# Performance work log

Hardware: AMD Instinct MI355X
Metric: run time of the kernel (lower is better)

The kernel has to match this reference:

```python
import jax, jax.numpy as jnp
import numpy as np
jax.config.update("jax_enable_x64", True)

HASH_PRIMES = [2654435761, 2246822519, 3266489917, 2028178513, 1220703125, 1610612741, 805306457, 402653189, 3674653429, 2860486313, 1073676287, 2971215073, 1500450271, 3267000013, 2654435789, 4049292737, 2246822531, 3266489927, 2028178519, 1220703133, 1610612743, 805306459, 402653191, 3674653433]
NUM_TABLES = 32
BUCKETS = 4096
VOCAB = 1024
BYTE_DIM = 256
EMBED_PER_TABLE = 8
HIDDEN = 512
N_BLOCKS = 3  # num_layers - 1
BATCH, SEQ = 32, 2048

def _generate_skip_patterns(num_tables):
    patterns = []
    for offset in range(1, min(num_tables // 4 + 1, 9)):
        patterns.append((offset,))
    pairs = [(1,2),(2,3),(3,4),(1,3),(2,4),(1,4),(1,5),(2,5),(3,5),(1,6),(2,6),(1,7)]
    for p in pairs:
        if len(patterns) >= num_tables:
            break
        patterns.append(p)
    trigrams = [(1,2,3),(1,2,4),(1,3,5),(2,3,4),(1,2,5),(1,3,4),(2,4,6),(1,4,7)]
    for t in trigrams:
        if len(patterns) >= num_tables:
            break
        patterns.append(t)
    offset = 8
    while len(patterns) < num_tables:
        patterns.append((1, offset))
        offset += 1
    return tuple(patterns[:num_tables])

SKIP_PATTERNS = _generate_skip_patterns(NUM_TABLES)

def _soft_hash(tokens, table_idx):
    # tokens: [B,S] int64. Faithful to torch: h = h ^ (shifted*prime);
    # h2 = h ^ ((h*prime2) >> 16)  (python precedence: * > >> > ^)
    B, S = tokens.shape
    pattern = SKIP_PATTERNS[table_idx]
    h = jnp.zeros((B, S), dtype=jnp.int64)
    for k, offset in enumerate(pattern):
        prime = HASH_PRIMES[(table_idx * 3 + k) % len(HASH_PRIMES)]
        shifted = jnp.zeros_like(tokens)
        if offset < S:
            shifted = shifted.at[:, offset:].set(tokens[:, :S - offset])
        h = h ^ (shifted * jnp.int64(prime))
    idx_lo = h % BUCKETS
    sp = HASH_PRIMES[(table_idx * 3 + len(pattern)) % len(HASH_PRIMES)]
    h2 = h ^ ((h * jnp.int64(sp)) >> 16)
    idx_hi = h2 % BUCKETS
    frac = (((h >> 3) & 255).astype(jnp.float32) / 255.0) * 0.4
    return idx_lo, idx_hi, frac

def setup_inputs() -> dict:
    key = jax.random.key(0)
    ks = jax.random.split(key, 8)
    chars = jax.random.randint(ks[0], (BATCH, SEQ), 0, VOCAB, dtype=jnp.int64)
    byte_embed = jax.random.normal(ks[1], (VOCAB, BYTE_DIM), dtype=jnp.float32)
    hash_tables = 0.02 * jax.random.normal(ks[2], (NUM_TABLES, BUCKETS, EMBED_PER_TABLE), dtype=jnp.float32)
    s_in = float(np.sqrt(6.0 / (HIDDEN + HIDDEN)))
    w_in = jax.random.uniform(ks[3], (HIDDEN, HIDDEN), jnp.float32, -s_in, s_in)
    b_in = jnp.zeros((HIDDEN,), jnp.float32)
    mlp_ws = jax.random.uniform(ks[4], (N_BLOCKS, HIDDEN, HIDDEN), jnp.float32, -s_in, s_in)
    mlp_bs = jnp.zeros((N_BLOCKS, HIDDEN), jnp.float32)
    s_out = float(np.sqrt(6.0 / (HIDDEN + VOCAB)))
    w_out = jax.random.uniform(ks[5], (VOCAB, HIDDEN), jnp.float32, -s_out, s_out)
    b_out = jnp.zeros((VOCAB,), jnp.float32)
    return {"chars": chars, "byte_embed": byte_embed, "hash_tables": hash_tables,
            "w_in": w_in, "b_in": b_in, "mlp_ws": mlp_ws, "mlp_bs": mlp_bs,
            "w_out": w_out, "b_out": b_out}

def reference(chars, byte_embed, hash_tables, w_in, b_in, mlp_ws, mlp_bs, w_out, b_out):
    # chars: [B,S] int64 -> logits [B,S,V]
    parts = [byte_embed[chars]]  # [B,S,256]
    for i in range(NUM_TABLES):
        idx_lo, idx_hi, frac = _soft_hash(chars, i)
        tab = hash_tables[i]                      # [BUCKETS, 8]
        frac = frac[..., None]                    # [B,S,1]
        emb = tab[idx_lo] * (1.0 - frac) + tab[idx_hi] * frac
        parts.append(emb)
    features = jnp.concatenate(parts, axis=-1)    # [B,S,512]
    h = jax.nn.relu(features @ w_in.T + b_in)
    for j in range(N_BLOCKS):
        # ResidualBlock: relu(linear(x)) + x (no layernorm/dropout in config)
        h = jax.nn.relu(h @ mlp_ws[j].T + mlp_bs[j]) + h
    logits = h @ w_out.T + b_out                  # [B,S,VOCAB]
    return logits
```

## Files before the change

### kernel.cpp

```cpp
#include <hip/hip_runtime.h>
#include <cstdint>
#include <cstddef>

typedef unsigned short u16;
typedef __attribute__((ext_vector_type(8))) short short8;
typedef __attribute__((ext_vector_type(4))) float f32x4;

#define NTOK 65536
#define HID 512
#define NVOCAB 1024

__device__ __forceinline__ u16 f2bf(float f) {
  union { float f; uint32_t u; } v; v.f = f;
  uint32_t r = (v.u + 0x7FFFu + ((v.u >> 16) & 1u)) >> 16;
  return (u16)r;
}
__device__ __forceinline__ float bf2f(u16 b) {
  union { uint32_t u; float f; } v; v.u = ((uint32_t)b) << 16;
  return v.f;
}

__constant__ uint32_t P24[24] = {
  2654435761u, 2246822519u, 3266489917u, 2028178513u, 1220703125u,
  1610612741u, 805306457u, 402653189u, 3674653429u, 2860486313u,
  1073676287u, 2971215073u, 1500450271u, 3267000013u, 2654435789u,
  4049292737u, 2246822531u, 3266489927u, 2028178519u, 1220703133u,
  1610612743u, 805306459u, 402653191u, 3674653433u};
__constant__ unsigned char OFFS[32][3] = {
  {1,0,0},{2,0,0},{3,0,0},{4,0,0},{5,0,0},{6,0,0},{7,0,0},{8,0,0},
  {1,2,0},{2,3,0},{3,4,0},{1,3,0},{2,4,0},{1,4,0},{1,5,0},{2,5,0},
  {3,5,0},{1,6,0},{2,6,0},{1,7,0},
  {1,2,3},{1,2,4},{1,3,5},{2,3,4},{1,2,5},{1,3,4},{2,4,6},{1,4,7},
  {1,8,0},{1,9,0},{1,10,0},{1,11,0}};
__constant__ unsigned char PLEN[32] = {
  1,1,1,1,1,1,1,1, 2,2,2,2,2,2,2,2,2,2,2,2, 3,3,3,3,3,3,3,3, 2,2,2,2};

__global__ __launch_bounds__(256) void pack_w(
    const float* __restrict__ w_in, const float* __restrict__ mlp_ws,
    const float* __restrict__ w_out, u16* __restrict__ Wp)
{
  const int gid  = blockIdx.x * 256 + threadIdx.x;
  const int L    = gid >> 15;
  const int c    = gid & 32767;
  const int lane = c & 63;
  const int ni   = (c >> 6) & 3;
  const int kk   = (c >> 8) & 15;
  const int w    = c >> 12;
  const float* base =
      (L == 0) ? w_in :
      (L <= 3) ? mlp_ws + (size_t)(L - 1) * 262144 :
                 w_out  + (size_t)(L - 4) * 262144;
  const int row = (w << 6) + (ni << 4) + (lane & 15);
  const int col = (kk << 5) + ((lane >> 4) << 3);
  const float* s = base + (size_t)row * 512 + col;
  float4 f0 = ((const float4*)s)[0];
  float4 f1 = ((const float4*)s)[1];
  short8 o;
  o[0]=(short)f2bf(f0.x); o[1]=(short)f2bf(f0.y); o[2]=(short)f2bf(f0.z); o[3]=(short)f2bf(f0.w);
  o[4]=(short)f2bf(f1.x); o[5]=(short)f2bf(f1.y); o[6]=(short)f2bf(f1.z); o[7]=(short)f2bf(f1.w);
  *(short8*)(Wp + (size_t)gid * 8) = o;
}

__global__ __launch_bounds__(512, 4)
void fused_all(const int* __restrict__ chars, const float* __restrict__ byte_embed,
               const float* __restrict__ hash_tables, const u16* __restrict__ Wp,
               const float* __restrict__ bIn, const float* __restrict__ bMlp,
               const float* __restrict__ bOut, float* __restrict__ out)
{
  __shared__ __align__(16) u16 hbuf[64 * 512];
  const int tid  = threadIdx.x;
  const int w    = tid >> 6;
  const int lane = tid & 63;
  const int g    = lane >> 4;
  const int lr   = lane & 15;
  const size_t tok0 = (size_t)blockIdx.x << 6;
  const int swz = (lr & 7) << 3;

  {
    const int sub = tid & 31;
    const int tl  = tid >> 5;
    const int i   = sub;
    const int pl  = (int)PLEN[i];
    #pragma unroll 1
    for (int pass = 0; pass < 4; ++pass) {
      const int tr = (pass << 4) + tl;
      const size_t t = tok0 + tr;
      const int pos = (int)(t & 2047);
      const int c = chars[t];
      const int sw = (tr & 7) << 3;
      {
        const float* src = byte_embed + ((size_t)c << 8) + (sub << 3);
        float4 f0 = ((const float4*)src)[0];
        float4 f1 = ((const float4*)src)[1];
        short8 o;
        o[0]=(short)f2bf(f0.x); o[1]=(short)f2bf(f0.y); o[2]=(short)f2bf(f0.z); o[3]=(short)f2bf(f0.w);
        o[4]=(short)f2bf(f1.x); o[5]=(short)f2bf(f1.y); o[6]=(short)f2bf(f1.z); o[7]=(short)f2bf(f1.w);
        *(short8*)&hbuf[(tr << 9) + (((sub << 3)) ^ sw)] = o;
      }
      {
        long long hv = 0;
        #pragma unroll
        for (int k = 0; k < 3; ++k) {
          if (k < pl) {
            const int off = (int)OFFS[i][k];
            const long long tok = (pos >= off) ? (long long)chars[t - off] : 0ll;
            hv ^= tok * (long long)P24[(3 * i + k) % 24];
          }
        }
        const int idx_lo = (int)(hv & 4095);
        const long long p2 = (long long)P24[(3 * i + pl) % 24];
        const long long prod = (long long)((unsigned long long)hv * (unsigned long long)p2);
        const long long h2 = hv ^ (prod >> 16);
        const int idx_hi = (int)(h2 & 4095);
        const float frac = ((float)(int)((hv >> 3) & 255) / 255.0f) * 0.4f;
        const float om = 1.0f - frac;
        const float* plo = hash_tables + (((size_t)i << 12) + (size_t)idx_lo) * 8;
        const float* phi = hash_tables + (((size_t)i << 12) + (size_t)idx_hi) * 8;
        float4 a0 = ((const float4*)plo)[0], a1 = ((const float4*)plo)[1];
        float4 b0 = ((const float4*)phi)[0], b1 = ((const float4*)phi)[1];
        short8 o;
        o[0]=(short)f2bf(a0.x*om + b0.x*frac); o[1]=(short)f2bf(a0.y*om + b0.y*frac);
        o[2]=(short)f2bf(a0.z*om + b0.z*frac); o[3]=(short)f2bf(a0.w*om + b0.w*frac);
        o[4]=(short)f2bf(a1.x*om + b1.x*frac); o[5]=(short)f2bf(a1.y*om + b1.y*frac);
        o[6]=(short)f2bf(a1.z*om + b1.z*frac); o[7]=(short)f2bf(a1.w*om + b1.w*frac);
        *(short8*)&hbuf[(tr << 9) + (((256 + (sub << 3))) ^ sw)] = o;
      }
    }
  }
  __syncthreads();

  f32x4 acc[4][4];

  auto gemm = [&](int L) {
    #pragma unroll
    for (int ni = 0; ni < 4; ++ni)
      #pragma unroll
      for (int ti = 0; ti < 4; ++ti) acc[ni][ti] = (f32x4){0.f, 0.f, 0.f, 0.f};
    const u16* Wl = Wp + (size_t)L * 262144 + (w << 15) + (lane << 3);
    #pragma unroll
    for (int kk = 0; kk < 16; ++kk) {
      short8 Wf[4], hf[4];
      #pragma unroll
      for (int ni = 0; ni < 4; ++ni)
        Wf[ni] = *(const short8*)(Wl + (kk << 11) + (ni << 9));
      const int kb = ((kk << 5) + (g << 3)) ^ swz;
      #pragma unroll
      for (int ti = 0; ti < 4; ++ti)
        hf[ti] = *(const short8*)&hbuf[(((ti << 4) + lr) << 9) + kb];
      #pragma unroll
      for (int ni = 0; ni < 4; ++ni)
        #pragma unroll
        for (int ti = 0; ti < 4; ++ti)
          acc[ni][ti] = __builtin_amdgcn_mfma_f32_16x16x32_bf16(Wf[ni], hf[ti], acc[ni][ti], 0, 0, 0);
    }
  };

  auto epi_h = [&](const float* __restrict__ bias, bool resid) {
    __syncthreads();
    #pragma unroll
    for (int ni = 0; ni < 4; ++ni) {
      const int nb = (w << 6) + (ni << 4) + (g << 2);
      const float4 b4 = *(const float4*)(bias + nb);
      #pragma unroll
      for (int ti = 0; ti < 4; ++ti) {
        const int t = (ti << 4) + lr;
        u16* p = &hbuf[(t << 9) + (nb ^ swz)];
        float v0 = fmaxf(acc[ni][ti][0] + b4.x, 0.f);
        float v1 = fmaxf(acc[ni][ti][1] + b4.y, 0.f);
        float v2 = fmaxf(acc[ni][ti][2] + b4.z, 0.f);
        float v3 = fmaxf(acc[ni][ti][3] + b4.w, 0.f);
        if (resid) {
          const uint2 r2 = *(const uint2*)p;
          v0 += bf2f((u16)(r2.x & 0xffffu)); v1 += bf2f((u16)(r2.x >> 16));
          v2 += bf2f((u16)(r2.y & 0xffffu)); v3 += bf2f((u16)(r2.y >> 16));
        }
        uint2 o;
        o.x = (uint32_t)f2bf(v0) | ((uint32_t)f2bf(v1) << 16);
        o.y = (uint32_t)f2bf(v2) | ((uint32_t)f2bf(v3) << 16);
        *(uint2*)p = o;
      }
    }
    __syncthreads();
  };

  auto epi_out = [&](const float* __restrict__ bias, int vb) {
    #pragma unroll
    for (int ni = 0; ni < 4; ++ni) {
      const int nb = (w << 6) + (ni << 4) + (g << 2);
      const float4 b4 = *(const float4*)(bias + nb);
      #pragma unroll
      for (int ti = 0; ti < 4; ++ti) {
        const int t = (ti << 4) + lr;
        float4 o;
        o.x = acc[ni][ti][0] + b4.x;
        o.y = acc[ni][ti][1] + b4.y;
        o.z = acc[ni][ti][2] + b4.z;
        o.w = acc[ni][ti][3] + b4.w;
        *(float4*)(out + (tok0 + t) * NVOCAB + vb + nb) = o;
      }
    }
  };

  gemm(0); epi_h(bIn, false);
  gemm(1); epi_h(bMlp,        true);
  gemm(2); epi_h(bMlp + 512,  true);
  gemm(3); epi_h(bMlp + 1024, true);
  gemm(4); epi_out(bOut,       0);
  gemm(5); epi_out(bOut + 512, 512);
}

extern "C" void kernel_launch(void* const* d_in, const int* in_sizes, int n_in,
                              void* d_out, int out_size, void* d_ws, size_t ws_size,
                              hipStream_t stream) {
  const int*   chars      = (const int*)  d_in[0];
  const float* byte_embed = (const float*)d_in[1];
  const float* hash_tabs  = (const float*)d_in[2];
  const float* w_in       = (const float*)d_in[3];
  const float* b_in       = (const float*)d_in[4];
  const float* mlp_ws     = (const float*)d_in[5];
  const float* mlp_bs     = (const float*)d_in[6];
  const float* w_out      = (const float*)d_in[7];
  const float* b_out      = (const float*)d_in[8];

  u16* Wp = (u16*)d_ws;

  pack_w<<<dim3(768), dim3(256), 0, stream>>>(w_in, mlp_ws, w_out, Wp);

  fused_all<<<dim3(NTOK / 64), dim3(512), 0, stream>>>(
      chars, byte_embed, hash_tabs, Wp, b_in, mlp_bs, b_out, (float*)d_out);
}
```

Measured before the change: 525.1 us.

## Persistent 1024-thread blocks with double-buffered feature prefetch overlapping GEMMs

Switches to 256 persistent blocks of 1024 threads, each handling four 64-token tiles. The feature gather for the next tile goes into a second LDS buffer while the output GEMMs of the current tile run. Each wave now owns 32 output columns instead of 64, and the weight packing layout is changed to match. MFMA sections are wrapped in s_setprio. The aim is to hide gather latency and raise wave count per CU, at the cost of 128KB of LDS per block, one block per CU, and less weight reuse per wave.

```diff
diff --git a/kernel.cpp b/kernel.cpp
--- a/kernel.cpp
+++ b/kernel.cpp
@@ -43,14 +43,14 @@
   const int L    = gid >> 15;
   const int c    = gid & 32767;
   const int lane = c & 63;
-  const int ni   = (c >> 6) & 3;
-  const int kk   = (c >> 8) & 15;
-  const int w    = c >> 12;
+  const int ni   = (c >> 6) & 1;
+  const int kk   = (c >> 7) & 15;
+  const int w    = c >> 11;
   const float* base =
       (L == 0) ? w_in :
       (L <= 3) ? mlp_ws + (size_t)(L - 1) * 262144 :
                  w_out  + (size_t)(L - 4) * 262144;
-  const int row = (w << 6) + (ni << 4) + (lane & 15);
+  const int row = (w << 5) + (ni << 4) + (lane & 15);
   const int col = (kk << 5) + ((lane >> 4) << 3);
   const float* s = base + (size_t)row * 512 + col;
   float4 f0 = ((const float4*)s)[0];
@@ -61,132 +61,128 @@
   *(short8*)(Wp + (size_t)gid * 8) = o;
 }
 
-__global__ __launch_bounds__(512, 4)
+__global__ __launch_bounds__(1024, 4)
 void fused_all(const int* __restrict__ chars, const float* __restrict__ byte_embed,
                const float* __restrict__ hash_tables, const u16* __restrict__ Wp,
                const float* __restrict__ bIn, const float* __restrict__ bMlp,
                const float* __restrict__ bOut, float* __restrict__ out)
 {
-  __shared__ __align__(16) u16 hbuf[64 * 512];
+  __shared__ __align__(16) u16 hh[2][64 * 512];
   const int tid  = threadIdx.x;
   const int w    = tid >> 6;
   const int lane = tid & 63;
   const int g    = lane >> 4;
   const int lr   = lane & 15;
-  const size_t tok0 = (size_t)blockIdx.x << 6;
-  const int swz = (lr & 7) << 3;
-
-  {
-    const int sub = tid & 31;
-    const int tl  = tid >> 5;
-    const int i   = sub;
-    const int pl  = (int)PLEN[i];
-    #pragma unroll 1
-    for (int pass = 0; pass < 4; ++pass) {
-      const int tr = (pass << 4) + tl;
-      const size_t t = tok0 + tr;
-      const int pos = (int)(t & 2047);
-      const int c = chars[t];
-      const int sw = (tr & 7) << 3;
-      {
-        const float* src = byte_embed + ((size_t)c << 8) + (sub << 3);
-        float4 f0 = ((const float4*)src)[0];
-        float4 f1 = ((const float4*)src)[1];
-        short8 o;
-        o[0]=(short)f2bf(f0.x); o[1]=(short)f2bf(f0.y); o[2]=(short)f2bf(f0.z); o[3]=(short)f2bf(f0.w);
-        o[4]=(short)f2bf(f1.x); o[5]=(short)f2bf(f1.y); o[6]=(short)f2bf(f1.z); o[7]=(short)f2bf(f1.w);
-        *(short8*)&hbuf[(tr << 9) + (((sub << 3)) ^ sw)] = o;
+  const int swz  = (lr & 7) << 3;
+  const int sub  = tid & 31;
+  const int tl   = tid >> 5;
+  const int pl   = (int)PLEN[sub];
+
+  f32x4 acc[2][4];
+  float4 G0, G1, G2, G3, G4, G5;
+  float  frS;
+
+  auto feat_issue = [&](size_t tok0t, int p) {
+    const int tr = (p << 5) + tl;
+    const size_t t = tok0t + tr;
+    const int pos = (int)(t & 2047);
+    const int c = chars[t];
+    long long hv = 0;
+    #pragma unroll
+    for (int k = 0; k < 3; ++k) {
+      if (k < pl) {
+        const int off = (int)OFFS[sub][k];
+        const long long tok = (pos >= off) ? (long long)chars[t - off] : 0ll;
+        hv ^= tok * (long long)P24[(3 * sub + k) % 24];
       }
-      {
-        long long hv = 0;
+    }
+    const int idx_lo = (int)(hv & 4095);
+    const long long sp = (long long)P24[(3 * sub + pl) % 24];
+    const long long prod = (long long)((unsigned long long)hv * (unsigned long long)sp);
+    const int idx_hi = (int)((hv ^ (prod >> 16)) & 4095);
+    frS = ((float)(int)((hv >> 3) & 255) / 255.0f) * 0.4f;
+    const float* plo = hash_tables + (((size_t)sub << 12) + (size_t)idx_lo) * 8;
+    const float* phi = hash_tables + (((size_t)sub << 12) + (size_t)idx_hi) * 8;
+    const float* pby = byte_embed + ((size_t)c << 8) + (sub << 3);
+    G0 = ((const float4*)plo)[0]; G1 = ((const float4*)plo)[1];
+    G2 = ((const float4*)phi)[0]; G3 = ((const float4*)phi)[1];
+    G4 = ((const float4*)pby)[0]; G5 = ((const float4*)pby)[1];
+  };
+  auto feat_consume = [&](u16* hb, int p) {
+    const int tr = (p << 5) + tl;
+    const int sw = (tr & 7) << 3;
+    short8 ob;
+    ob[0]=(short)f2bf(G4.x); ob[1]=(short)f2bf(G4.y); ob[2]=(short)f2bf(G4.z); ob[3]=(short)f2bf(G4.w);
+    ob[4]=(short)f2bf(G5.x); ob[5]=(short)f2bf(G5.y); ob[6]=(short)f2bf(G5.z); ob[7]=(short)f2bf(G5.w);
+    *(short8*)&hb[(tr << 9) + ((sub << 3) ^ sw)] = ob;
+    const float fr = frS, om = 1.0f - fr;
+    short8 oh;
+    oh[0]=(short)f2bf(G0.x*om + G2.x*fr); oh[1]=(short)f2bf(G0.y*om + G2.y*fr);
+    oh[2]=(short)f2bf(G0.z*om + G2.z*fr); oh[3]=(short)f2bf(G0.w*om + G2.w*fr);
+    oh[4]=(short)f2bf(G1.x*om + G3.x*fr); oh[5]=(short)f2bf(G1.y*om + G3.y*fr);
+    oh[6]=(short)f2bf(G1.z*om + G3.z*fr); oh[7]=(short)f2bf(G1.w*om + G3.w*fr);
+    *(short8*)&hb[(tr << 9) + ((256 + (sub << 3)) ^ sw)] = oh;
+  };
+
+  auto gemm = [&](int L, const u16* hb, int kk0, int kk1, bool zero) {
+    if (zero) {
+      #pragma unroll
+      for (int ni = 0; ni < 2; ++ni)
         #pragma unroll
-        for (int k = 0; k < 3; ++k) {
-          if (k < pl) {
-            const int off = (int)OFFS[i][k];
-            const long long tok = (pos >= off) ? (long long)chars[t - off] : 0ll;
-            hv ^= tok * (long long)P24[(3 * i + k) % 24];
-          }
-        }
-        const int idx_lo = (int)(hv & 4095);
-        const long long p2 = (long long)P24[(3 * i + pl) % 24];
-        const long long prod = (long long)((unsigned long long)hv * (unsigned long long)p2);
-        const long long h2 = hv ^ (prod >> 16);
-        const int idx_hi = (int)(h2 & 4095);
-        const float frac = ((float)(int)((hv >> 3) & 255) / 255.0f) * 0.4f;
-        const float om = 1.0f - frac;
-        const float* plo = hash_tables + (((size_t)i << 12) + (size_t)idx_lo) * 8;
-        const float* phi = hash_tables + (((size_t)i << 12) + (size_t)idx_hi) * 8;
-        float4 a0 = ((const float4*)plo)[0], a1 = ((const float4*)plo)[1];
-        float4 b0 = ((const float4*)phi)[0], b1 = ((const float4*)phi)[1];
-        short8 o;
-        o[0]=(short)f2bf(a0.x*om + b0.x*frac); o[1]=(short)f2bf(a0.y*om + b0.y*frac);
-        o[2]=(short)f2bf(a0.z*om + b0.z*frac); o[3]=(short)f2bf(a0.w*om + b0.w*frac);
-        o[4]=(short)f2bf(a1.x*om + b1.x*frac); o[5]=(short)f2bf(a1.y*om + b1.y*frac);
-        o[6]=(short)f2bf(a1.z*om + b1.z*frac); o[7]=(short)f2bf(a1.w*om + b1.w*frac);
-        *(short8*)&hbuf[(tr << 9) + (((256 + (sub << 3))) ^ sw)] = o;
-      }
-    }
-  }
-  __syncthreads();
-
-  f32x4 acc[4][4];
-
-  auto gemm = [&](int L) {
-    #pragma unroll
-    for (int ni = 0; ni < 4; ++ni)
-      #pragma unroll
-      for (int ti = 0; ti < 4; ++ti) acc[ni][ti] = (f32x4){0.f, 0.f, 0.f, 0.f};
-    const u16* Wl = Wp + (size_t)L * 262144 + (w << 15) + (lane << 3);
-    #pragma unroll
-    for (int kk = 0; kk < 16; ++kk) {
-      short8 Wf[4], hf[4];
-      #pragma unroll
-      for (int ni = 0; ni < 4; ++ni)
-        Wf[ni] = *(const short8*)(Wl + (kk << 11) + (ni << 9));
+        for (int ti = 0; ti < 4; ++ti) acc[ni][ti] = (f32x4){0.f, 0.f, 0.f, 0.f};
+    }
+    const u16* Wl = Wp + (size_t)L * 262144 + (w << 14) + (lane << 3);
+    #pragma unroll
+    for (int kk = kk0; kk < kk1; ++kk) {
+      short8 Wf[2], hf[4];
+      Wf[0] = *(const short8*)(Wl + (kk << 10));
+      Wf[1] = *(const short8*)(Wl + (kk << 10) + 512);
       const int kb = ((kk << 5) + (g << 3)) ^ swz;
       #pragma unroll
       for (int ti = 0; ti < 4; ++ti)
-        hf[ti] = *(const short8*)&hbuf[(((ti << 4) + lr) << 9) + kb];
-      #pragma unroll
-      for (int ni = 0; ni < 4; ++ni)
+        hf[ti] = *(const short8*)&hb[(((ti << 4) + lr) << 9) + kb];
+      __builtin_amdgcn_s_setprio(1);
+      #pragma unroll
+      for (int ni = 0; ni < 2; ++ni)
         #pragma unroll
         for (int ti = 0; ti < 4; ++ti)
           acc[ni][ti] = __builtin_amdgcn_mfma_f32_16x16x32_bf16(Wf[ni], hf[ti], acc[ni][ti], 0, 0, 0);
-    }
-  };
-
-  auto epi_h = [&](const float* __restrict__ bias, bool resid) {
+      __builtin_amdgcn_s_setprio(0);
+    }
+  };
+
+  auto epi_h = [&](const float* __restrict__ bias, bool resid, u16* hb) {
     __syncthreads();
     #pragma unroll
-    for (int ni = 0; ni < 4; ++ni) {
-      const int nb = (w << 6) + (ni << 4) + (g << 2);
+    for (int ni = 0; ni < 2; ++ni) {
+      const int nb = (w << 5) + (ni << 4) + (g << 2);
       const float4 b4 = *(const float4*)(bias + nb);
       #pragma unroll
       for (int ti = 0; ti < 4; ++ti) {
         const int t = (ti << 4) + lr;
-        u16* p = &hbuf[(t << 9) + (nb ^ swz)];
+        u16* pp = &hb[(t << 9) + (nb ^ swz)];
         float v0 = fmaxf(acc[ni][ti][0] + b4.x, 0.f);
         float v1 = fmaxf(acc[ni][ti][1] + b4.y, 0.f);
         float v2 = fmaxf(acc[ni][ti][2] + b4.z, 0.f);
         float v3 = fmaxf(acc[ni][ti][3] + b4.w, 0.f);
         if (resid) {
-          const uint2 r2 = *(const uint2*)p;
+          const uint2 r2 = *(const uint2*)pp;
           v0 += bf2f((u16)(r2.x & 0xffffu)); v1 += bf2f((u16)(r2.x >> 16));
           v2 += bf2f((u16)(r2.y & 0xffffu)); v3 += bf2f((u16)(r2.y >> 16));
         }
         uint2 o;
         o.x = (uint32_t)f2bf(v0) | ((uint32_t)f2bf(v1) << 16);
         o.y = (uint32_t)f2bf(v2) | ((uint32_t)f2bf(v3) << 16);
-        *(uint2*)p = o;
+        *(uint2*)pp = o;
       }
     }
     __syncthreads();
   };
 
-  auto epi_out = [&](const float* __restrict__ bias, int vb) {
-    #pragma unroll
-    for (int ni = 0; ni < 4; ++ni) {
-      const int nb = (w << 6) + (ni << 4) + (g << 2);
+  auto epi_out = [&](const float* __restrict__ bias, int vb, size_t tok0t) {
+    #pragma unroll
+    for (int ni = 0; ni < 2; ++ni) {
+      const int nb = (w << 5) + (ni << 4) + (g << 2);
       const float4 b4 = *(const float4*)(bias + nb);
       #pragma unroll
       for (int ti = 0; ti < 4; ++ti) {
@@ -196,17 +192,46 @@
         o.y = acc[ni][ti][1] + b4.y;
         o.z = acc[ni][ti][2] + b4.z;
         o.w = acc[ni][ti][3] + b4.w;
-        *(float4*)(out + (tok0 + t) * NVOCAB + vb + nb) = o;
+        *(float4*)(out + (tok0t + t) * NVOCAB + vb + nb) = o;
       }
     }
   };
 
-  gemm(0); epi_h(bIn, false);
-  gemm(1); epi_h(bMlp,        true);
-  gemm(2); epi_h(bMlp + 512,  true);
-  gemm(3); epi_h(bMlp + 1024, true);
-  gemm(4); epi_out(bOut,       0);
-  gemm(5); epi_out(bOut + 512, 512);
+  const size_t base = (size_t)blockIdx.x << 8;
+
+  feat_issue(base, 0); feat_consume(hh[0], 0);
+  feat_issue(base, 1); feat_consume(hh[0], 1);
+  __syncthreads();
+
+  #pragma unroll 1
+  for (int j = 0; j < 4; ++j) {
+    u16* hc = hh[j & 1];
+    u16* hn = hh[(j & 1) ^ 1];
+    const size_t tk0 = base + ((size_t)j << 6);
+    const bool more = (j < 3);
+
+    gemm(0, hc, 0, 16, true);  epi_h(bIn,         false, hc);
+    gemm(1, hc, 0, 16, true);  epi_h(bMlp,        true,  hc);
+    gemm(2, hc, 0, 16, true);  epi_h(bMlp + 512,  true,  hc);
+    gemm(3, hc, 0, 16, true);  epi_h(bMlp + 1024, true,  hc);
+
+    if (more) {
+      gemm(4, hc, 0, 8, true);
+      feat_issue(tk0 + 64, 0);
+      gemm(4, hc, 8, 16, false);
+      feat_consume(hn, 0);
+      feat_issue(tk0 + 64, 1);
+      epi_out(bOut, 0, tk0);
+      gemm(5, hc, 0, 8, true);
+      feat_consume(hn, 1);
+      gemm(5, hc, 8, 16, false);
+      epi_out(bOut + 512, 512, tk0);
+      __syncthreads();
+    } else {
+      gemm(4, hc, 0, 16, true);  epi_out(bOut,       0,   tk0);
+      gemm(5, hc, 0, 16, true);  epi_out(bOut + 512, 512, tk0);
+    }
+  }
 }
 
 extern "C" void kernel_launch(void* const* d_in, const int* in_sizes, int n_in,
@@ -226,6 +251,6 @@
 
   pack_w<<<dim3(768), dim3(256), 0, stream>>>(w_in, mlp_ws, w_out, Wp);
 
-  fused_all<<<dim3(NTOK / 64), dim3(512), 0, stream>>>(
+  fused_all<<<dim3(256), dim3(1024), 0, stream>>>(
       chars, byte_embed, hash_tabs, Wp, b_in, mlp_bs, b_out, (float*)d_out);
 }
```

Result: slower. 1.325 ms (+152.3%).
